# Performance work log

Measured on AMD Instinct MI355X. Metric: run time of the kernel, lower is better.

## Reference

```python
import jax, jax.numpy as jnp
import numpy as np

NUM_RAYS = 262144   # 512x512 rays
LENGTH = 128        # path_length
NUM_LEAVES = 1048576
MAX_DIST = 1e10
EPS = 1e-10


def setup_inputs() -> dict:
    key = jax.random.key(0)
    k1, k2, k3 = jax.random.split(key, 3)
    # t_stops must be increasing along each ray
    t_stops = jnp.sort(jax.random.uniform(k1, (NUM_RAYS, LENGTH), jnp.float32, 0.0, 4.0), axis=-1)
    leaves = jax.random.randint(k2, (NUM_RAYS, LENGTH), 0, NUM_LEAVES, dtype=jnp.int64)
    logits = jax.random.normal(k3, (NUM_LEAVES,), jnp.float32) - 10.0  # init near -10 like the module
    return {"t_stops": t_stops, "leaves": leaves, "logits": logits}


def reference(t_stops, leaves, logits):
    num_rays, length = leaves.shape
    # gather per-sample opacity
    opacity = jax.nn.sigmoid(logits)[leaves]                      # [R, L]
    # segment lengths; last segment extends to "infinity"
    deltas = jnp.concatenate(
        [t_stops[:, 1:] - t_stops[:, :-1],
         jnp.full((num_rays, 1), MAX_DIST, dtype=t_stops.dtype)], axis=-1)
    alpha = 1.0 - jnp.exp(-(opacity * deltas))                    # [R, L]
    trans = jnp.minimum(1.0, 1.0 - alpha + EPS)
    # shift right: transmittance before first sample is 1
    trans = jnp.concatenate(
        [jnp.ones((num_rays, 1), dtype=alpha.dtype), trans[:, 1:]], axis=-1)
    weights = alpha * jnp.cumprod(trans, axis=-1)                 # [R, L]
    return weights.sum(axis=-1)                                   # [R]
```

## Files before the change

kernel.cpp:

```cpp
#include <hip/hip_runtime.h>
#include <hip/hip_fp16.h>
#include <math.h>


#define NRAYS 262144
#define LEN   128
#define NLEAF 1048576
#define MAXD  1e10f
#define EPSW  1e-10f

typedef float v4f __attribute__((ext_vector_type(4)));
typedef int   v4i __attribute__((ext_vector_type(4)));

__device__ __forceinline__ float fast_sigmoid(float x) {
    return __builtin_amdgcn_rcpf(1.0f + __expf(-x));
}

__device__ __forceinline__ float omexp(float x) {
    float p = x * (1.0f + x * (-0.5f + x * (0.16666667f - 0.041666668f * x)));
    return (x < 0.1f) ? p : (1.0f - __expf(-x));
}

__device__ __forceinline__ float tab_gather32(const unsigned int* tb32, int idx) {
    unsigned int v = tb32[idx >> 1];
    unsigned short u = (unsigned short)(v >> ((idx & 1) * 16));
    __half h;
    *(unsigned short*)&h = u;
    return __half2float(h);
}

__global__ __launch_bounds__(256) void sig_kernel(const float* __restrict__ logits,
                                                  __half* __restrict__ tab) {
    int i = blockIdx.x * 256 + threadIdx.x;
    tab[i] = __float2half(fast_sigmoid(logits[i]));
}

template <bool TAB>
__global__ __launch_bounds__(256) void vc_kernel(
    const float* __restrict__ t_stops,
    const int*   __restrict__ leaves,
    const void*  __restrict__ table,
    float*       __restrict__ out)
{
    const int lane = threadIdx.x & 63;
    const int wid  = blockIdx.x * 4 + (threadIdx.x >> 6);
    const int ray  = wid * 8 + (lane >> 3);
    const int sub  = lane & 7;
    const int gbase = lane & 56;

    const long long rb = (long long)ray * LEN + sub * 4;

    v4i lv[4];
    v4f tt[4];
    #pragma unroll
    for (int c = 0; c < 4; ++c)
        lv[c] = __builtin_nontemporal_load((const v4i*)(leaves + rb + c * 32));
    #pragma unroll
    for (int c = 0; c < 4; ++c)
        tt[c] = __builtin_nontemporal_load((const v4f*)(t_stops + rb + c * 32));

    float op[4][4];
    if (TAB) {
        const unsigned int* tb32 = (const unsigned int*)table;
        #pragma unroll
        for (int c = 0; c < 4; ++c) {
            op[c][0] = tab_gather32(tb32, lv[c].x);
            op[c][1] = tab_gather32(tb32, lv[c].y);
            op[c][2] = tab_gather32(tb32, lv[c].z);
            op[c][3] = tab_gather32(tb32, lv[c].w);
        }
    } else {
        const float* lg = (const float*)table;
        #pragma unroll
        for (int c = 0; c < 4; ++c) {
            op[c][0] = fast_sigmoid(lg[lv[c].x]);
            op[c][1] = fast_sigmoid(lg[lv[c].y]);
            op[c][2] = fast_sigmoid(lg[lv[c].z]);
            op[c][3] = fast_sigmoid(lg[lv[c].w]);
        }
    }

    float P[4], S[4];
    #pragma unroll
    for (int c = 0; c < 4; ++c) {
        float nxt_dn = __shfl_down(tt[c].x, 1);
        float nxt_c1 = (c < 3) ? __shfl(tt[(c + 1) & 3].x, gbase) : MAXD;
        float nxt = (sub == 7) ? nxt_c1 : nxt_dn;

        float d0 = tt[c].y - tt[c].x;
        float d1 = tt[c].z - tt[c].y;
        float d2 = tt[c].w - tt[c].z;
        float d3 = nxt - tt[c].w;

        float a0 = omexp(op[c][0] * d0);
        float a1 = omexp(op[c][1] * d1);
        float a2 = omexp(op[c][2] * d2);
        float a3 = omexp(op[c][3] * d3);

        float r0 = fminf(1.0f, 1.0f - a0 + EPSW);
        float r1 = fminf(1.0f, 1.0f - a1 + EPSW);
        float r2 = fminf(1.0f, 1.0f - a2 + EPSW);
        float r3 = fminf(1.0f, 1.0f - a3 + EPSW);
        if (c == 0 && sub == 0) r0 = 1.0f;

        float cc = r0;        float ss = a0 * cc;
        cc *= r1;             ss = fmaf(a1, cc, ss);
        cc *= r2;             ss = fmaf(a2, cc, ss);
        cc *= r3;             ss = fmaf(a3, cc, ss);
        P[c] = cc;  S[c] = ss;
    }

    #pragma unroll
    for (int o = 1; o < 8; o <<= 1) {
        #pragma unroll
        for (int c = 0; c < 4; ++c) {
            float Pp = __shfl_xor(P[c], o);
            float Sp = __shfl_xor(S[c], o);
            S[c] = (lane & o) ? fmaf(Pp, S[c], Sp) : fmaf(P[c], Sp, S[c]);
            P[c] *= Pp;
        }
    }

    float Sr = fmaf(P[2], S[3], S[2]);
    Sr = fmaf(P[1], Sr, S[1]);
    Sr = fmaf(P[0], Sr, S[0]);

    if (sub == 0)
        out[ray] = Sr;
}

extern "C" void kernel_launch(void* const* d_in, const int* in_sizes, int n_in,
                              void* d_out, int out_size, void* d_ws, size_t ws_size,
                              hipStream_t stream) {
    const float* t_stops = (const float*)d_in[0];
    const int*   leaves  = (const int*)d_in[1];
    const float* logits  = (const float*)d_in[2];
    float*       out     = (float*)d_out;

    if (ws_size >= NLEAF * sizeof(__half)) {
        sig_kernel<<<NLEAF / 256, 256, 0, stream>>>(logits, (__half*)d_ws);
        vc_kernel<true><<<NRAYS / 32, 256, 0, stream>>>(t_stops, leaves, d_ws, out);
    } else {
        vc_kernel<false><<<NRAYS / 32, 256, 0, stream>>>(t_stops, leaves, logits, out);
    }
}
```

Baseline: 368.1 us.

## Software-pipeline ray groups per wave with prefetched leaves and gathers

Each wavefront now handles 8 groups of 8 rays instead of one. Loads and table gathers for the next group are issued while the current group is computed, with leaf indices fetched two groups ahead, and the grid shrinks by 8x. The aim is to hide the latency of the dependent load-then-gather chain inside a single wave instead of relying on many resident waves. In exchange it uses more registers for double buffers and launches far fewer waves, which could reduce memory-level parallelism.

```diff
diff --git a/kernel.cpp b/kernel.cpp
--- a/kernel.cpp
+++ b/kernel.cpp
@@ -8,6 +8,7 @@
 #define NLEAF 1048576
 #define MAXD  1e10f
 #define EPSW  1e-10f
+#define GPW   8
 
 typedef float v4f __attribute__((ext_vector_type(4)));
 typedef int   v4i __attribute__((ext_vector_type(4)));
@@ -36,30 +37,8 @@
 }
 
 template <bool TAB>
-__global__ __launch_bounds__(256) void vc_kernel(
-    const float* __restrict__ t_stops,
-    const int*   __restrict__ leaves,
-    const void*  __restrict__ table,
-    float*       __restrict__ out)
-{
-    const int lane = threadIdx.x & 63;
-    const int wid  = blockIdx.x * 4 + (threadIdx.x >> 6);
-    const int ray  = wid * 8 + (lane >> 3);
-    const int sub  = lane & 7;
-    const int gbase = lane & 56;
-
-    const long long rb = (long long)ray * LEN + sub * 4;
-
-    v4i lv[4];
-    v4f tt[4];
-    #pragma unroll
-    for (int c = 0; c < 4; ++c)
-        lv[c] = __builtin_nontemporal_load((const v4i*)(leaves + rb + c * 32));
-    #pragma unroll
-    for (int c = 0; c < 4; ++c)
-        tt[c] = __builtin_nontemporal_load((const v4f*)(t_stops + rb + c * 32));
-
-    float op[4][4];
+__device__ __forceinline__ void do_gather(const void* __restrict__ table,
+                                          const v4i lv[4], float op[4][4]) {
     if (TAB) {
         const unsigned int* tb32 = (const unsigned int*)table;
         #pragma unroll
@@ -79,7 +58,10 @@
             op[c][3] = fast_sigmoid(lg[lv[c].w]);
         }
     }
+}
 
+__device__ __forceinline__ float compute_ray(const v4f tt[4], const float op[4][4],
+                                             int lane, int sub, int gbase) {
     float P[4], S[4];
     #pragma unroll
     for (int c = 0; c < 4; ++c) {
@@ -124,9 +106,72 @@
     float Sr = fmaf(P[2], S[3], S[2]);
     Sr = fmaf(P[1], Sr, S[1]);
     Sr = fmaf(P[0], Sr, S[0]);
+    return Sr;
+}
 
+template <bool TAB, int IT>
+__device__ __forceinline__ void pipe_step(
+    const float* __restrict__ t_stops, const int* __restrict__ leaves,
+    const void* __restrict__ table, float* __restrict__ out,
+    v4i lv[4], const v4f ttc[4], v4f ttn[4],
+    const float opc[4][4], float opn[4][4],
+    int eb0, int w, int lane, int sub, int gbase)
+{
+    if (IT + 1 < GPW) {
+        do_gather<TAB>(table, lv, opn);
+        #pragma unroll
+        for (int c = 0; c < 4; ++c)
+            ttn[c] = __builtin_nontemporal_load(
+                (const v4f*)(t_stops + eb0 + (IT + 1) * 1024 + c * 32));
+        if (IT + 2 < GPW) {
+            #pragma unroll
+            for (int c = 0; c < 4; ++c)
+                lv[c] = __builtin_nontemporal_load(
+                    (const v4i*)(leaves + eb0 + (IT + 2) * 1024 + c * 32));
+        }
+    }
+    float Sr = compute_ray(ttc, opc, lane, sub, gbase);
     if (sub == 0)
-        out[ray] = Sr;
+        out[(w * GPW + IT) * 8 + (lane >> 3)] = Sr;
+}
+
+template <bool TAB>
+__global__ __launch_bounds__(256) void vc_kernel(
+    const float* __restrict__ t_stops,
+    const int*   __restrict__ leaves,
+    const void*  __restrict__ table,
+    float*       __restrict__ out)
+{
+    const int lane  = threadIdx.x & 63;
+    const int sub   = lane & 7;
+    const int gbase = lane & 56;
+    const int w     = blockIdx.x * 4 + (threadIdx.x >> 6);
+
+    const int eb0 = (w * GPW * 8 + (lane >> 3)) * LEN + sub * 4;
+
+    v4i  lv[4];
+    v4f  tt[2][4];
+    float op[2][4][4];
+
+    #pragma unroll
+    for (int c = 0; c < 4; ++c)
+        lv[c] = __builtin_nontemporal_load((const v4i*)(leaves + eb0 + c * 32));
+    #pragma unroll
+    for (int c = 0; c < 4; ++c)
+        tt[0][c] = __builtin_nontemporal_load((const v4f*)(t_stops + eb0 + c * 32));
+    do_gather<TAB>(table, lv, op[0]);
+    #pragma unroll
+    for (int c = 0; c < 4; ++c)
+        lv[c] = __builtin_nontemporal_load((const v4i*)(leaves + eb0 + 1024 + c * 32));
+
+    pipe_step<TAB, 0>(t_stops, leaves, table, out, lv, tt[0], tt[1], op[0], op[1], eb0, w, lane, sub, gbase);
+    pipe_step<TAB, 1>(t_stops, leaves, table, out, lv, tt[1], tt[0], op[1], op[0], eb0, w, lane, sub, gbase);
+    pipe_step<TAB, 2>(t_stops, leaves, table, out, lv, tt[0], tt[1], op[0], op[1], eb0, w, lane, sub, gbase);
+    pipe_step<TAB, 3>(t_stops, leaves, table, out, lv, tt[1], tt[0], op[1], op[0], eb0, w, lane, sub, gbase);
+    pipe_step<TAB, 4>(t_stops, leaves, table, out, lv, tt[0], tt[1], op[0], op[1], eb0, w, lane, sub, gbase);
+    pipe_step<TAB, 5>(t_stops, leaves, table, out, lv, tt[1], tt[0], op[1], op[0], eb0, w, lane, sub, gbase);
+    pipe_step<TAB, 6>(t_stops, leaves, table, out, lv, tt[0], tt[1], op[0], op[1], eb0, w, lane, sub, gbase);
+    pipe_step<TAB, 7>(t_stops, leaves, table, out, lv, tt[1], tt[0], op[1], op[0], eb0, w, lane, sub, gbase);
 }
 
 extern "C" void kernel_launch(void* const* d_in, const int* in_sizes, int n_in,
@@ -139,8 +184,8 @@
 
     if (ws_size >= NLEAF * sizeof(__half)) {
         sig_kernel<<<NLEAF / 256, 256, 0, stream>>>(logits, (__half*)d_ws);
-        vc_kernel<true><<<NRAYS / 32, 256, 0, stream>>>(t_stops, leaves, d_ws, out);
+        vc_kernel<true><<<NRAYS / 256, 256, 0, stream>>>(t_stops, leaves, d_ws, out);
     } else {
-        vc_kernel<false><<<NRAYS / 32, 256, 0, stream>>>(t_stops, leaves, logits, out);
+        vc_kernel<false><<<NRAYS / 256, 256, 0, stream>>>(t_stops, leaves, logits, out);
     }
 }
```

After: 373.2 us. No clear change (+1.4%).
